# Optimization experiments

Measured on AMD Instinct MI355X. Metric: run time of the kernel, lower is better.

## Reference

```python
import jax, jax.numpy as jnp
import numpy as np

DEPTH, LENGTH, WIDTH, NUM_CLASSES = 8, 32, 32, 8
STD_POSITION = 1.0
STD_INTENSITY = 3.0


def setup_inputs() -> dict:
    key = jax.random.key(0)
    k1, k2 = jax.random.split(key)
    patch = jax.random.normal(k1, (DEPTH, LENGTH, WIDTH), dtype=jnp.float32)
    prob = jax.random.uniform(k2, (DEPTH, LENGTH, WIDTH, NUM_CLASSES), dtype=jnp.float32)
    return {"patch": patch, "prob": prob, "k": NUM_CLASSES}


def _dist_weight():
    # Matches torch.meshgrid(arange(depth), arange(length), arange(width)) with 'ij' indexing,
    # then row-major flatten. dist_weight[i,j] = exp(-||pos_i - pos_j||^2 / std_position^2)
    gx, gy, gz = jnp.meshgrid(
        jnp.arange(DEPTH, dtype=jnp.float32),
        jnp.arange(LENGTH, dtype=jnp.float32),
        jnp.arange(WIDTH, dtype=jnp.float32),
        indexing="ij",
    )
    x, y, z = gx.ravel(), gy.ravel(), gz.ravel()  # each [n]
    sq = (
        jnp.square(x[:, None] - x[None, :])
        + jnp.square(y[:, None] - y[None, :])
        + jnp.square(z[:, None] - z[None, :])
    )  # [n, n]
    return jnp.exp(-sq / (STD_POSITION ** 2))


def reference(patch, prob, k):
    n = DEPTH * LENGTH * WIDTH
    f = patch.reshape(-1)  # [n]
    # intensity_weight is .detach()ed in the original -> stop_gradient for faithfulness
    intensity = jax.lax.stop_gradient(
        jnp.exp(-jnp.square((f[:, None] - f[None, :]) / STD_INTENSITY))
    )  # [n, n]
    W = intensity * _dist_weight()  # [n, n]

    P = prob.reshape(n, k)  # row-major flatten matches torch.reshape of prob[:,:,:,t]
    WP = W @ P  # [n, k]
    num = jnp.sum(P * WP, axis=0)            # per-class p^T W p
    den = P.T @ (W @ jnp.ones((n,), W.dtype))  # per-class p^T W 1
    loss = jnp.float32(k) - jnp.sum(num / den)
    return loss.astype(jnp.float32)
```

## Files before the change

kernel.cpp:

```cpp
#include <hip/hip_runtime.h>

#define N        8192
#define NCLS     8
#define QUADS    2048
#define WAVES_PB 8
#define TPB      512
#define GRID     (QUADS / WAVES_PB)
#define GROUPS   16
#define GPB      (GRID / GROUPS)

#define L1_DW    16384
#define L2_DW    16896
#define BASE_DW  16960

__global__ __launch_bounds__(TPB, 2) void sncut_fused(const float* __restrict__ f,
                                                      const float* __restrict__ P,
                                                      float* __restrict__ ws,
                                                      float* __restrict__ out)
{
    const int tid  = threadIdx.x;
    const int lane = tid & 63;
    const int wave = tid >> 6;
    const int q    = blockIdx.x * WAVES_PB + wave;

    const int xi  = q >> 8;
    const int rem = q & 255;
    const int yi  = (rem >> 4) << 1;
    const int zi  = (rem & 15) << 1;

    const int ibase = (xi << 10) + (yi << 5) + zi;
    const float fi00 = f[ibase];
    const float fi01 = f[ibase + 1];
    const float fi10 = f[ibase + 32];
    const float fi11 = f[ibase + 33];

    int Y0 = yi - 3; Y0 = Y0 < 0 ? 0 : (Y0 > 24 ? 24 : Y0);
    int Z0 = zi - 3; Z0 = Z0 < 0 ? 0 : (Z0 > 24 ? 24 : Z0);
    int X0 = xi - 3; X0 = X0 < 0 ? 0 : (X0 > 1 ? 1 : X0);

    const int oy = lane >> 3, oz = lane & 7;
    const int yj = Y0 + oy, zj = Z0 + oz;
    const int jcol = (yj << 5) + zj;

    const float dy0 = (float)(yi - yj),     dy1 = (float)(yi + 1 - yj);
    const float dz0 = (float)(zi - zj),     dz1 = (float)(zi + 1 - zj);
    const float b00 = dy0 * dy0 + dz0 * dz0;
    const float b01 = dy0 * dy0 + dz1 * dz1;
    const float b10 = dy1 * dy1 + dz0 * dz0;
    const float b11 = dy1 * dy1 + dz1 * dz1;

    float  fjv[7];
    float4 p0v[7], p1v[7];
    #pragma unroll
    for (int k = 0; k < 7; ++k) {
        const int j = ((X0 + k) << 10) + jcol;
        fjv[k] = f[j];
        p0v[k] = *reinterpret_cast<const float4*>(P + (size_t)j * NCLS);
        p1v[k] = *reinterpret_cast<const float4*>(P + (size_t)j * NCLS + 4);
    }

    float vv[4][9];
    #pragma unroll
    for (int c = 0; c < 4; ++c)
        #pragma unroll
        for (int t = 0; t < 9; ++t) vv[c][t] = 0.f;

    #pragma unroll
    for (int k = 0; k < 7; ++k) {
        const int dx = xi - (X0 + k);
        const float dx2 = (float)(dx * dx);
        const float fj  = fjv[k];
        const float4 p0 = p0v[k];
        const float4 p1 = p1v[k];

        float df, w;
        df = fi00 - fj; w = __expf(-(df * df * (1.0f / 9.0f) + b00 + dx2));
        vv[0][0] += w * p0.x; vv[0][1] += w * p0.y; vv[0][2] += w * p0.z; vv[0][3] += w * p0.w;
        vv[0][4] += w * p1.x; vv[0][5] += w * p1.y; vv[0][6] += w * p1.z; vv[0][7] += w * p1.w;
        vv[0][8] += w;
        df = fi01 - fj; w = __expf(-(df * df * (1.0f / 9.0f) + b01 + dx2));
        vv[1][0] += w * p0.x; vv[1][1] += w * p0.y; vv[1][2] += w * p0.z; vv[1][3] += w * p0.w;
        vv[1][4] += w * p1.x; vv[1][5] += w * p1.y; vv[1][6] += w * p1.z; vv[1][7] += w * p1.w;
        vv[1][8] += w;
        df = fi10 - fj; w = __expf(-(df * df * (1.0f / 9.0f) + b10 + dx2));
        vv[2][0] += w * p0.x; vv[2][1] += w * p0.y; vv[2][2] += w * p0.z; vv[2][3] += w * p0.w;
        vv[2][4] += w * p1.x; vv[2][5] += w * p1.y; vv[2][6] += w * p1.z; vv[2][7] += w * p1.w;
        vv[2][8] += w;
        df = fi11 - fj; w = __expf(-(df * df * (1.0f / 9.0f) + b11 + dx2));
        vv[3][0] += w * p0.x; vv[3][1] += w * p0.y; vv[3][2] += w * p0.z; vv[3][3] += w * p0.w;
        vv[3][4] += w * p1.x; vv[3][5] += w * p1.y; vv[3][6] += w * p1.z; vv[3][7] += w * p1.w;
        vv[3][8] += w;
    }

    float4 pc0[4], pc1[4];
    if (lane == 0) {
        const int ic[4] = {ibase, ibase + 1, ibase + 32, ibase + 33};
        #pragma unroll
        for (int c = 0; c < 4; ++c) {
            pc0[c] = *reinterpret_cast<const float4*>(P + (size_t)ic[c] * NCLS);
            pc1[c] = *reinterpret_cast<const float4*>(P + (size_t)ic[c] * NCLS + 4);
        }
    }

    #pragma unroll
    for (int c = 0; c < 4; ++c)
        #pragma unroll
        for (int t = 0; t < 9; ++t) {
            float x = vv[c][t];
            #pragma unroll
            for (int off = 32; off > 0; off >>= 1)
                x += __shfl_down(x, off, 64);
            vv[c][t] = x;
        }

    __shared__ float sh[WAVES_PB][16];
    if (lane == 0) {
        float r16[16];
        #pragma unroll
        for (int e = 0; e < 16; ++e) r16[e] = 0.f;
        #pragma unroll
        for (int c = 0; c < 4; ++c) {
            r16[0]  += pc0[c].x * vv[c][0];
            r16[1]  += pc0[c].y * vv[c][1];
            r16[2]  += pc0[c].z * vv[c][2];
            r16[3]  += pc0[c].w * vv[c][3];
            r16[4]  += pc1[c].x * vv[c][4];
            r16[5]  += pc1[c].y * vv[c][5];
            r16[6]  += pc1[c].z * vv[c][6];
            r16[7]  += pc1[c].w * vv[c][7];
            r16[8]  += pc0[c].x * vv[c][8];
            r16[9]  += pc0[c].y * vv[c][8];
            r16[10] += pc0[c].z * vv[c][8];
            r16[11] += pc0[c].w * vv[c][8];
            r16[12] += pc1[c].x * vv[c][8];
            r16[13] += pc1[c].y * vv[c][8];
            r16[14] += pc1[c].z * vv[c][8];
            r16[15] += pc1[c].w * vv[c][8];
        }
        #pragma unroll
        for (int e = 0; e < 16; ++e) sh[wave][e] = r16[e];
    }
    __syncthreads();
    if (tid < 16) {
        float s = 0.f;
        #pragma unroll
        for (int wv = 0; wv < WAVES_PB; ++wv) s += sh[wv][tid];
        __hip_atomic_store(&ws[(size_t)blockIdx.x * 16 + tid], s,
                           __ATOMIC_RELAXED, __HIP_MEMORY_SCOPE_AGENT);
    }

    __shared__ int isLast;
    __syncthreads();
    if (tid == 0) {
        unsigned int* w32 = (unsigned int*)ws;
        const unsigned int base =
            __hip_atomic_load(w32 + BASE_DW, __ATOMIC_RELAXED, __HIP_MEMORY_SCOPE_AGENT);
        const int grp = blockIdx.x >> 4;
        const unsigned int o1 =
            __hip_atomic_fetch_add(w32 + L1_DW + grp * 32, 1u,
                                   __ATOMIC_RELAXED, __HIP_MEMORY_SCOPE_AGENT);
        int last = 0;
        if (((o1 - base) & (unsigned int)(GPB - 1)) == (unsigned int)(GPB - 1)) {
            const unsigned int o2 =
                __hip_atomic_fetch_add(w32 + L2_DW, 1u,
                                       __ATOMIC_RELAXED, __HIP_MEMORY_SCOPE_AGENT);
            last = (((o2 - base) & (unsigned int)(GROUPS - 1)) == (unsigned int)(GROUPS - 1));
        }
        isLast = last;
    }
    __syncthreads();
    if (!isLast) return;

    const int e = tid & 15;
    const int g = tid >> 4;
    float s2 = 0.f;
    #pragma unroll
    for (int m = 0; m < GRID / 32; ++m)
        s2 += __hip_atomic_load(&ws[(size_t)(g + m * 32) * 16 + e],
                                __ATOMIC_RELAXED, __HIP_MEMORY_SCOPE_AGENT);

    __shared__ float acc2[32][17];
    acc2[g][e] = s2;
    __syncthreads();

    __shared__ float sums[16];
    if (tid < 16) {
        float t = 0.f;
        #pragma unroll
        for (int g2 = 0; g2 < 32; ++g2) t += acc2[g2][tid];
        sums[tid] = t;
    }
    __syncthreads();
    if (tid == 0) {
        float loss = (float)NCLS;
        #pragma unroll
        for (int t = 0; t < NCLS; ++t) loss -= sums[t] / sums[NCLS + t];
        out[0] = loss;
    }
}

extern "C" void kernel_launch(void* const* d_in, const int* in_sizes, int n_in,
                              void* d_out, int out_size, void* d_ws, size_t ws_size,
                              hipStream_t stream) {
    const float* f = (const float*)d_in[0];
    const float* P = (const float*)d_in[1];

    sncut_fused<<<GRID, TPB, 0, stream>>>(f, P, (float*)d_ws, (float*)d_out);
}
```

Measured before the change: 63.85 us.

## Reuse neighbor column loads across four x-planes per single-wave block

Each single-wave block now handles one (y,z) 2x2 quad across four consecutive x planes, reusing the 7 loaded neighbor values of f and P for all four planes instead of reloading them per plane. Per-lane partial sums are projected onto the center P before the cross-lane reduction, so only 16 values are shuffle-reduced per wave instead of 36. The block-level shared-memory reductions and syncthreads are replaced by a two-level last-block scheme done entirely with wave shuffles. In exchange the grid shrinks to 512 single-wave blocks, which raises register pressure and lowers parallelism per block.

```diff
diff --git a/kernel.cpp b/kernel.cpp
--- a/kernel.cpp
+++ b/kernel.cpp
@@ -2,52 +2,35 @@
 
 #define N        8192
 #define NCLS     8
-#define QUADS    2048
-#define WAVES_PB 8
-#define TPB      512
-#define GRID     (QUADS / WAVES_PB)
-#define GROUPS   16
+#define TPB      64
+#define GRID     512
+#define GROUPS   32
 #define GPB      (GRID / GROUPS)
 
+#define GP_DW    8192
 #define L1_DW    16384
-#define L2_DW    16896
-#define BASE_DW  16960
+#define L2_DW    17472
+#define BASE_DW  17536
 
-__global__ __launch_bounds__(TPB, 2) void sncut_fused(const float* __restrict__ f,
-                                                      const float* __restrict__ P,
-                                                      float* __restrict__ ws,
-                                                      float* __restrict__ out)
+__global__ __launch_bounds__(TPB) void sncut_fused(const float* __restrict__ f,
+                                                   const float* __restrict__ P,
+                                                   float* __restrict__ ws,
+                                                   float* __restrict__ out)
 {
-    const int tid  = threadIdx.x;
-    const int lane = tid & 63;
-    const int wave = tid >> 6;
-    const int q    = blockIdx.x * WAVES_PB + wave;
-
-    const int xi  = q >> 8;
-    const int rem = q & 255;
-    const int yi  = (rem >> 4) << 1;
-    const int zi  = (rem & 15) << 1;
-
-    const int ibase = (xi << 10) + (yi << 5) + zi;
-    const float fi00 = f[ibase];
-    const float fi01 = f[ibase + 1];
-    const float fi10 = f[ibase + 32];
-    const float fi11 = f[ibase + 33];
+    const int lane = threadIdx.x;
+    const int b    = blockIdx.x;
+    const int half = b >> 8;
+    const int rem  = b & 255;
+    const int yi   = ((rem >> 4) & 15) << 1;
+    const int zi   = (rem & 15) << 1;
 
     int Y0 = yi - 3; Y0 = Y0 < 0 ? 0 : (Y0 > 24 ? 24 : Y0);
     int Z0 = zi - 3; Z0 = Z0 < 0 ? 0 : (Z0 > 24 ? 24 : Z0);
-    int X0 = xi - 3; X0 = X0 < 0 ? 0 : (X0 > 1 ? 1 : X0);
+    const int X0 = half;
 
     const int oy = lane >> 3, oz = lane & 7;
     const int yj = Y0 + oy, zj = Z0 + oz;
     const int jcol = (yj << 5) + zj;
-
-    const float dy0 = (float)(yi - yj),     dy1 = (float)(yi + 1 - yj);
-    const float dz0 = (float)(zi - zj),     dz1 = (float)(zi + 1 - zj);
-    const float b00 = dy0 * dy0 + dz0 * dz0;
-    const float b01 = dy0 * dy0 + dz1 * dz1;
-    const float b10 = dy1 * dy1 + dz0 * dz0;
-    const float b11 = dy1 * dy1 + dz1 * dz1;
 
     float  fjv[7];
     float4 p0v[7], p1v[7];
@@ -59,144 +42,134 @@
         p1v[k] = *reinterpret_cast<const float4*>(P + (size_t)j * NCLS + 4);
     }
 
-    float vv[4][9];
+    float fic[4][4];
     #pragma unroll
-    for (int c = 0; c < 4; ++c)
-        #pragma unroll
-        for (int t = 0; t < 9; ++t) vv[c][t] = 0.f;
+    for (int cx = 0; cx < 4; ++cx) {
+        const int ib = ((half * 4 + cx) << 10) + (yi << 5) + zi;
+        fic[cx][0] = f[ib];      fic[cx][1] = f[ib + 1];
+        fic[cx][2] = f[ib + 32]; fic[cx][3] = f[ib + 33];
+    }
+
+    const float dy0 = (float)(yi - yj),     dy1 = (float)(yi + 1 - yj);
+    const float dz0 = (float)(zi - zj),     dz1 = (float)(zi + 1 - zj);
+    const float byz[4] = { dy0 * dy0 + dz0 * dz0, dy0 * dy0 + dz1 * dz1,
+                           dy1 * dy1 + dz0 * dz0, dy1 * dy1 + dz1 * dz1 };
+
+    float r16[16];
+    #pragma unroll
+    for (int e = 0; e < 16; ++e) r16[e] = 0.f;
 
     #pragma unroll
-    for (int k = 0; k < 7; ++k) {
-        const int dx = xi - (X0 + k);
-        const float dx2 = (float)(dx * dx);
-        const float fj  = fjv[k];
-        const float4 p0 = p0v[k];
-        const float4 p1 = p1v[k];
+    for (int cx = 0; cx < 4; ++cx) {
+        float vv[4][9];
+        #pragma unroll
+        for (int c = 0; c < 4; ++c)
+            #pragma unroll
+            for (int t = 0; t < 9; ++t) vv[c][t] = 0.f;
 
-        float df, w;
-        df = fi00 - fj; w = __expf(-(df * df * (1.0f / 9.0f) + b00 + dx2));
-        vv[0][0] += w * p0.x; vv[0][1] += w * p0.y; vv[0][2] += w * p0.z; vv[0][3] += w * p0.w;
-        vv[0][4] += w * p1.x; vv[0][5] += w * p1.y; vv[0][6] += w * p1.z; vv[0][7] += w * p1.w;
-        vv[0][8] += w;
-        df = fi01 - fj; w = __expf(-(df * df * (1.0f / 9.0f) + b01 + dx2));
-        vv[1][0] += w * p0.x; vv[1][1] += w * p0.y; vv[1][2] += w * p0.z; vv[1][3] += w * p0.w;
-        vv[1][4] += w * p1.x; vv[1][5] += w * p1.y; vv[1][6] += w * p1.z; vv[1][7] += w * p1.w;
-        vv[1][8] += w;
-        df = fi10 - fj; w = __expf(-(df * df * (1.0f / 9.0f) + b10 + dx2));
-        vv[2][0] += w * p0.x; vv[2][1] += w * p0.y; vv[2][2] += w * p0.z; vv[2][3] += w * p0.w;
-        vv[2][4] += w * p1.x; vv[2][5] += w * p1.y; vv[2][6] += w * p1.z; vv[2][7] += w * p1.w;
-        vv[2][8] += w;
-        df = fi11 - fj; w = __expf(-(df * df * (1.0f / 9.0f) + b11 + dx2));
-        vv[3][0] += w * p0.x; vv[3][1] += w * p0.y; vv[3][2] += w * p0.z; vv[3][3] += w * p0.w;
-        vv[3][4] += w * p1.x; vv[3][5] += w * p1.y; vv[3][6] += w * p1.z; vv[3][7] += w * p1.w;
-        vv[3][8] += w;
-    }
+        #pragma unroll
+        for (int k = 0; k < 7; ++k) {
+            const int dx = 3 * half + cx - k;
+            const float dx2 = (float)(dx * dx);
+            const float fj  = fjv[k];
+            const float4 p0 = p0v[k];
+            const float4 p1 = p1v[k];
+            #pragma unroll
+            for (int c = 0; c < 4; ++c) {
+                const float df = fic[cx][c] - fj;
+                const float w  = __expf(-(df * df * (1.0f / 9.0f) + byz[c] + dx2));
+                vv[c][0] += w * p0.x; vv[c][1] += w * p0.y;
+                vv[c][2] += w * p0.z; vv[c][3] += w * p0.w;
+                vv[c][4] += w * p1.x; vv[c][5] += w * p1.y;
+                vv[c][6] += w * p1.z; vv[c][7] += w * p1.w;
+                vv[c][8] += w;
+            }
+        }
 
-    float4 pc0[4], pc1[4];
-    if (lane == 0) {
-        const int ic[4] = {ibase, ibase + 1, ibase + 32, ibase + 33};
         #pragma unroll
         for (int c = 0; c < 4; ++c) {
-            pc0[c] = *reinterpret_cast<const float4*>(P + (size_t)ic[c] * NCLS);
-            pc1[c] = *reinterpret_cast<const float4*>(P + (size_t)ic[c] * NCLS + 4);
+            const int ic = ((half * 4 + cx) << 10) + ((yi + (c >> 1)) << 5) + (zi + (c & 1));
+            const float4 q0 = *reinterpret_cast<const float4*>(P + (size_t)ic * NCLS);
+            const float4 q1 = *reinterpret_cast<const float4*>(P + (size_t)ic * NCLS + 4);
+            r16[0]  += q0.x * vv[c][0]; r16[1]  += q0.y * vv[c][1];
+            r16[2]  += q0.z * vv[c][2]; r16[3]  += q0.w * vv[c][3];
+            r16[4]  += q1.x * vv[c][4]; r16[5]  += q1.y * vv[c][5];
+            r16[6]  += q1.z * vv[c][6]; r16[7]  += q1.w * vv[c][7];
+            r16[8]  += q0.x * vv[c][8]; r16[9]  += q0.y * vv[c][8];
+            r16[10] += q0.z * vv[c][8]; r16[11] += q0.w * vv[c][8];
+            r16[12] += q1.x * vv[c][8]; r16[13] += q1.y * vv[c][8];
+            r16[14] += q1.z * vv[c][8]; r16[15] += q1.w * vv[c][8];
         }
     }
 
     #pragma unroll
-    for (int c = 0; c < 4; ++c)
+    for (int e = 0; e < 16; ++e) {
+        float x = r16[e];
         #pragma unroll
-        for (int t = 0; t < 9; ++t) {
-            float x = vv[c][t];
-            #pragma unroll
-            for (int off = 32; off > 0; off >>= 1)
-                x += __shfl_down(x, off, 64);
-            vv[c][t] = x;
-        }
-
-    __shared__ float sh[WAVES_PB][16];
-    if (lane == 0) {
-        float r16[16];
-        #pragma unroll
-        for (int e = 0; e < 16; ++e) r16[e] = 0.f;
-        #pragma unroll
-        for (int c = 0; c < 4; ++c) {
-            r16[0]  += pc0[c].x * vv[c][0];
-            r16[1]  += pc0[c].y * vv[c][1];
-            r16[2]  += pc0[c].z * vv[c][2];
-            r16[3]  += pc0[c].w * vv[c][3];
-            r16[4]  += pc1[c].x * vv[c][4];
-            r16[5]  += pc1[c].y * vv[c][5];
-            r16[6]  += pc1[c].z * vv[c][6];
-            r16[7]  += pc1[c].w * vv[c][7];
-            r16[8]  += pc0[c].x * vv[c][8];
-            r16[9]  += pc0[c].y * vv[c][8];
-            r16[10] += pc0[c].z * vv[c][8];
-            r16[11] += pc0[c].w * vv[c][8];
-            r16[12] += pc1[c].x * vv[c][8];
-            r16[13] += pc1[c].y * vv[c][8];
-            r16[14] += pc1[c].z * vv[c][8];
-            r16[15] += pc1[c].w * vv[c][8];
-        }
-        #pragma unroll
-        for (int e = 0; e < 16; ++e) sh[wave][e] = r16[e];
-    }
-    __syncthreads();
-    if (tid < 16) {
-        float s = 0.f;
-        #pragma unroll
-        for (int wv = 0; wv < WAVES_PB; ++wv) s += sh[wv][tid];
-        __hip_atomic_store(&ws[(size_t)blockIdx.x * 16 + tid], s,
-                           __ATOMIC_RELAXED, __HIP_MEMORY_SCOPE_AGENT);
+        for (int off = 32; off > 0; off >>= 1)
+            x += __shfl_down(x, off, 64);
+        r16[e] = x;
     }
 
-    __shared__ int isLast;
-    __syncthreads();
-    if (tid == 0) {
+    if (lane == 0) {
+        #pragma unroll
+        for (int e = 0; e < 16; ++e)
+            __hip_atomic_store(&ws[(size_t)b * 16 + e], r16[e],
+                               __ATOMIC_RELAXED, __HIP_MEMORY_SCOPE_AGENT);
+    }
+    asm volatile("s_waitcnt vmcnt(0)" ::: "memory");
+
+    unsigned int pbase = 0u;
+    int fl = 0;
+    if (lane == 0) {
         unsigned int* w32 = (unsigned int*)ws;
-        const unsigned int base =
-            __hip_atomic_load(w32 + BASE_DW, __ATOMIC_RELAXED, __HIP_MEMORY_SCOPE_AGENT);
-        const int grp = blockIdx.x >> 4;
+        pbase = __hip_atomic_load(w32 + BASE_DW, __ATOMIC_RELAXED, __HIP_MEMORY_SCOPE_AGENT);
         const unsigned int o1 =
-            __hip_atomic_fetch_add(w32 + L1_DW + grp * 32, 1u,
+            __hip_atomic_fetch_add(w32 + L1_DW + (b >> 4) * 32, 1u,
                                    __ATOMIC_RELAXED, __HIP_MEMORY_SCOPE_AGENT);
-        int last = 0;
-        if (((o1 - base) & (unsigned int)(GPB - 1)) == (unsigned int)(GPB - 1)) {
-            const unsigned int o2 =
-                __hip_atomic_fetch_add(w32 + L2_DW, 1u,
-                                       __ATOMIC_RELAXED, __HIP_MEMORY_SCOPE_AGENT);
-            last = (((o2 - base) & (unsigned int)(GROUPS - 1)) == (unsigned int)(GROUPS - 1));
-        }
-        isLast = last;
+        fl = (((o1 - pbase) & (unsigned int)(GPB - 1)) == (unsigned int)(GPB - 1));
     }
-    __syncthreads();
-    if (!isLast) return;
+    fl = __shfl(fl, 0, 64);
+    if (!fl) return;
 
-    const int e = tid & 15;
-    const int g = tid >> 4;
+    const int grp = b >> 4;
+    const int e = lane & 15, q = lane >> 4;
+    float s = 0.f;
+    #pragma unroll
+    for (int mm = 0; mm < 4; ++mm)
+        s += __hip_atomic_load(&ws[(size_t)(grp * GPB + q + mm * 4) * 16 + e],
+                               __ATOMIC_RELAXED, __HIP_MEMORY_SCOPE_AGENT);
+    s += __shfl_down(s, 32, 64);
+    s += __shfl_down(s, 16, 64);
+    if (lane < 16)
+        __hip_atomic_store(&ws[GP_DW + (size_t)grp * 16 + lane], s,
+                           __ATOMIC_RELAXED, __HIP_MEMORY_SCOPE_AGENT);
+    asm volatile("s_waitcnt vmcnt(0)" ::: "memory");
+
+    int gl = 0;
+    if (lane == 0) {
+        unsigned int* w32 = (unsigned int*)ws;
+        const unsigned int o2 =
+            __hip_atomic_fetch_add(w32 + L2_DW, 1u,
+                                   __ATOMIC_RELAXED, __HIP_MEMORY_SCOPE_AGENT);
+        gl = (((o2 - pbase) & (unsigned int)(GROUPS - 1)) == (unsigned int)(GROUPS - 1));
+    }
+    gl = __shfl(gl, 0, 64);
+    if (!gl) return;
+
     float s2 = 0.f;
     #pragma unroll
-    for (int m = 0; m < GRID / 32; ++m)
-        s2 += __hip_atomic_load(&ws[(size_t)(g + m * 32) * 16 + e],
+    for (int mm = 0; mm < 8; ++mm)
+        s2 += __hip_atomic_load(&ws[GP_DW + (size_t)(q + mm * 4) * 16 + e],
                                 __ATOMIC_RELAXED, __HIP_MEMORY_SCOPE_AGENT);
+    s2 += __shfl_down(s2, 32, 64);
+    s2 += __shfl_down(s2, 16, 64);
 
-    __shared__ float acc2[32][17];
-    acc2[g][e] = s2;
-    __syncthreads();
-
-    __shared__ float sums[16];
-    if (tid < 16) {
-        float t = 0.f;
-        #pragma unroll
-        for (int g2 = 0; g2 < 32; ++g2) t += acc2[g2][tid];
-        sums[tid] = t;
-    }
-    __syncthreads();
-    if (tid == 0) {
-        float loss = (float)NCLS;
-        #pragma unroll
-        for (int t = 0; t < NCLS; ++t) loss -= sums[t] / sums[NCLS + t];
-        out[0] = loss;
-    }
+    float r = s2 / __shfl_down(s2, 8, 64);
+    r += __shfl_down(r, 4, 64);
+    r += __shfl_down(r, 2, 64);
+    r += __shfl_down(r, 1, 64);
+    if (lane == 0) out[0] = (float)NCLS - r;
 }
 
 extern "C" void kernel_launch(void* const* d_in, const int* in_sizes, int n_in,
```

After: 64.75 us. About the same (+1.4%).
